# Kernel optimization log

Hardware: AMD Instinct MI355X
Metric: run time of the kernel (lower is better)

Reference implementation:

```python
import jax, jax.numpy as jnp
import numpy as np


def _ternarize(p, delta, w):
    # {-w, 0, +w} via threshold mask, matching TrainableTernarize.forward
    return jnp.where(p > delta, w, jnp.where(p < -delta, -w, jnp.zeros_like(p)))


def _ternary_para(p, w):
    # TrainableTernaryPara.forward: delta = 0.05 * max|p|
    delta = 0.05 * jnp.max(jnp.abs(p))
    return _ternarize(p, delta, w)


def _init_scale(p):
    # w init: mean(|p|[|p| > 0.7 * mean|p|])
    a = jnp.abs(p)
    mask = (a > 0.7 * jnp.mean(a)).astype(p.dtype)
    return jnp.sum(a * mask) / jnp.sum(mask)


def setup_inputs() -> dict:
    key = jax.random.key(0)
    k1, k2, k3 = jax.random.split(key, 3)
    B, S, D_IN, D_OUT = 4, 2048, 4096, 4096
    x = jax.random.normal(k1, (B, S, D_IN), dtype=jnp.float32)
    bound = 1.0 / np.sqrt(D_IN)  # nn.Linear default init range
    W = jax.random.uniform(k2, (D_OUT, D_IN), minval=-bound, maxval=bound, dtype=jnp.float32)
    b = jax.random.uniform(k3, (D_OUT,), minval=-bound, maxval=bound, dtype=jnp.float32)
    w_scale = _init_scale(W)
    b_scale = _init_scale(b)
    return {"x": x, "W": W, "w_scale": w_scale, "b": b, "b_scale": b_scale}


def reference(x, W, w_scale, b, b_scale):
    Wt = _ternary_para(W, w_scale)   # [D_OUT, D_IN] in {-w,0,+w}
    bt = _ternary_para(b, b_scale)   # [D_OUT]
    # F.linear(x, Wt, bt) = x @ Wt.T + bt
    return jnp.einsum('bsi,oi->bso', x, Wt) + bt
```

## Files before the change

kernel.cpp:

```cpp
#include <hip/hip_runtime.h>

typedef int v4i __attribute__((ext_vector_type(4)));

#define BM 128
#define BN 128
#define BK 64

#define GLOAD_LDS(gptr, lptr)                                                         \
  __builtin_amdgcn_global_load_lds(                                                   \
      (const __attribute__((address_space(1))) unsigned int*)(gptr),                  \
      (__attribute__((address_space(3))) unsigned int*)(lptr), 16, 0, 0)


__global__ void absmax2_kernel(const float4* __restrict__ W4, long nW4,
                               const float4* __restrict__ b4, int nb4,
                               unsigned* __restrict__ mx) {
  __shared__ float sm[4];
  float m = 0.f;
  const bool isB = (blockIdx.x == gridDim.x - 1);
  if (!isB) {
    const long stride = (long)(gridDim.x - 1) * blockDim.x;
    for (long i = blockIdx.x * (long)blockDim.x + threadIdx.x; i < nW4; i += stride) {
      float4 v = W4[i];
      m = fmaxf(m, fmaxf(fmaxf(fabsf(v.x), fabsf(v.y)), fmaxf(fabsf(v.z), fabsf(v.w))));
    }
  } else {
    for (int i = threadIdx.x; i < nb4; i += blockDim.x) {
      float4 v = b4[i];
      m = fmaxf(m, fmaxf(fmaxf(fabsf(v.x), fabsf(v.y)), fmaxf(fabsf(v.z), fabsf(v.w))));
    }
  }
  for (int off = 32; off > 0; off >>= 1)
    m = fmaxf(m, __shfl_down(m, off));
  if ((threadIdx.x & 63) == 0) sm[threadIdx.x >> 6] = m;
  __syncthreads();
  if (threadIdx.x == 0) {
    m = fmaxf(fmaxf(sm[0], sm[1]), fmaxf(sm[2], sm[3]));
    atomicMax(mx + (isB ? 1 : 0), __float_as_uint(m));
  }
}

__global__ void xquant_kernel(const float4* __restrict__ X4,
                              signed char* __restrict__ Q,
                              float* __restrict__ sx, int K) {
  __shared__ float sm[4];
  const int row = blockIdx.x;
  const int tid = threadIdx.x;
  const float4* xr = X4 + (size_t)row * (K / 4);
  float4 v[4];
  float m = 0.f;
#pragma unroll
  for (int i = 0; i < 4; ++i) {
    v[i] = xr[tid * 4 + i];
    m = fmaxf(m, fmaxf(fmaxf(fabsf(v[i].x), fabsf(v[i].y)),
                       fmaxf(fabsf(v[i].z), fabsf(v[i].w))));
  }
  for (int off = 32; off > 0; off >>= 1) m = fmaxf(m, __shfl_down(m, off));
  if ((tid & 63) == 0) sm[tid >> 6] = m;
  __syncthreads();
  const float total = fmaxf(fmaxf(sm[0], sm[1]), fmaxf(sm[2], sm[3]));
  const float inv = 127.f / total;
  int wds[4];
#pragma unroll
  for (int i = 0; i < 4; ++i) {
    const float* f = (const float*)&v[i];
    int b[4];
#pragma unroll
    for (int j = 0; j < 4; ++j) {
      float r = rintf(f[j] * inv);
      r = fmaxf(-127.f, fminf(127.f, r));
      b[j] = ((int)r) & 255;
    }
    wds[i] = b[0] | (b[1] << 8) | (b[2] << 16) | (b[3] << 24);
  }
  v4i* out = (v4i*)(Q + (size_t)row * K);
  v4i o = {wds[0], wds[1], wds[2], wds[3]};
  out[tid] = o;
  if (tid == 0) sx[row] = total * (1.f / 127.f);
}

__global__ void prep_w_kernel(const float4* __restrict__ W4, long nW16,
                              const float4* __restrict__ b4, int nb4,
                              const unsigned* __restrict__ mx,
                              const float* __restrict__ bscale,
                              v4i* __restrict__ Tw, float4* __restrict__ bt) {
  if (blockIdx.x == gridDim.x - 1) {
    const float delta = 0.05f * __uint_as_float(mx[1]);
    const float s = *bscale;
    for (int i = threadIdx.x; i < nb4; i += blockDim.x) {
      float4 v = b4[i];
      float4 o;
      o.x = v.x > delta ? s : (v.x < -delta ? -s : 0.f);
      o.y = v.y > delta ? s : (v.y < -delta ? -s : 0.f);
      o.z = v.z > delta ? s : (v.z < -delta ? -s : 0.f);
      o.w = v.w > delta ? s : (v.w < -delta ? -s : 0.f);
      bt[i] = o;
    }
    return;
  }
  long i = blockIdx.x * (long)blockDim.x + threadIdx.x;
  if (i >= nW16) return;
  const float delta = 0.05f * __uint_as_float(mx[0]);
  int wds[4];
#pragma unroll
  for (int u = 0; u < 4; ++u) {
    float4 w = W4[i * 4 + u];
    int b0 = w.x > delta ? 1 : (w.x < -delta ? 0xFF : 0);
    int b1 = w.y > delta ? 1 : (w.y < -delta ? 0xFF : 0);
    int b2 = w.z > delta ? 1 : (w.z < -delta ? 0xFF : 0);
    int b3 = w.w > delta ? 1 : (w.w < -delta ? 0xFF : 0);
    wds[u] = b0 | (b1 << 8) | (b2 << 16) | (b3 << 24);
  }
  v4i o = {wds[0], wds[1], wds[2], wds[3]};
  Tw[i] = o;
}

__global__ __launch_bounds__(256) void gemm_tern_i8(
    const signed char* __restrict__ A,
    const signed char* __restrict__ B,
    const float* __restrict__ sx,
    const float* __restrict__ bt,
    const float* __restrict__ wsc,
    float* __restrict__ C,
    int M, int N, int K) {
  __shared__ __align__(16) signed char sA[BM * BK];
  __shared__ __align__(16) signed char sB[BN * BK];

  const int tid = threadIdx.x;
  const int wave = tid >> 6;
  const int lane = tid & 63;
  const int wm = wave >> 1, wn = wave & 1;
  const int quad = lane >> 4;
  const int l16 = lane & 15;

  const int bm0 = blockIdx.y * BM;
  const int bn0 = blockIdx.x * BN;

  const int srow = tid >> 2;
  const int scol = ((tid & 3) ^ ((tid >> 3) & 3)) * 16;

  const signed char* gA0 = A + (size_t)(bm0 + srow) * K + scol;
  const signed char* gA1 = A + (size_t)(bm0 + 64 + srow) * K + scol;
  const signed char* gB0 = B + (size_t)(bn0 + srow) * K + scol;
  const signed char* gB1 = B + (size_t)(bn0 + 64 + srow) * K + scol;

  signed char* lA0 = sA + (wave * 16) * BK;
  signed char* lA1 = sA + (64 + wave * 16) * BK;
  signed char* lB0 = sB + (wave * 16) * BK;
  signed char* lB1 = sB + (64 + wave * 16) * BK;

  const int kchunk = quad ^ ((l16 >> 1) & 3);
  const v4i* fA = (const v4i*)(sA + (wm * 64 + l16) * BK + kchunk * 16);
  const v4i* fB = (const v4i*)(sB + (wn * 64 + l16) * BK + kchunk * 16);

  v4i acc[4][4] = {};

  for (int k0 = 0; k0 < K; k0 += BK) {
    GLOAD_LDS(gA0, lA0);
    GLOAD_LDS(gA1, lA1);
    GLOAD_LDS(gB0, lB0);
    GLOAD_LDS(gB1, lB1);
    gA0 += BK; gA1 += BK; gB0 += BK; gB1 += BK;
    __syncthreads();

    v4i af[4], bfr[4];
#pragma unroll
    for (int i = 0; i < 4; ++i) af[i] = fA[i * 64];
#pragma unroll
    for (int i = 0; i < 4; ++i) bfr[i] = fB[i * 64];
#pragma unroll
    for (int mt = 0; mt < 4; ++mt)
#pragma unroll
      for (int nt = 0; nt < 4; ++nt)
        acc[mt][nt] = __builtin_amdgcn_mfma_i32_16x16x64_i8(
            af[mt], bfr[nt], acc[mt][nt], 0, 0, 0);
    __syncthreads();
  }

  const float ws = *wsc;
#pragma unroll
  for (int mt = 0; mt < 4; ++mt) {
    const int row = bm0 + wm * 64 + mt * 16 + quad * 4;
    float sc[4];
#pragma unroll
    for (int r = 0; r < 4; ++r) sc[r] = ws * sx[row + r];
#pragma unroll
    for (int nt = 0; nt < 4; ++nt) {
      const int col = bn0 + wn * 64 + nt * 16 + l16;
      const float bias = bt[col];
#pragma unroll
      for (int r = 0; r < 4; ++r)
        C[(size_t)(row + r) * N + col] = sc[r] * (float)acc[mt][nt][r] + bias;
    }
  }
}


extern "C" void kernel_launch(void* const* d_in, const int* in_sizes, int n_in,
                              void* d_out, int out_size, void* d_ws, size_t ws_size,
                              hipStream_t stream) {
  const float* x = (const float*)d_in[0];
  const float* W = (const float*)d_in[1];
  const float* w_scale = (const float*)d_in[2];
  const float* b = (const float*)d_in[3];
  const float* b_scale = (const float*)d_in[4];
  float* out = (float*)d_out;

  const int K = 4096;
  const int N = in_sizes[3];
  const int M = in_sizes[0] / K;

  char* ws = (char*)d_ws;
  signed char* xb = (signed char*)ws;
  signed char* Tw = (signed char*)(ws + (size_t)M * K);
  float* bt = (float*)(ws + (size_t)M * K + (size_t)N * K);
  float* sx = bt + N;
  unsigned* mx = (unsigned*)(sx + M);

  hipMemsetAsync(mx, 0, 8, stream);

  const long nW4 = (long)N * K / 4;
  const int nb4 = N / 4;

  absmax2_kernel<<<1025, 256, 0, stream>>>((const float4*)W, nW4,
                                           (const float4*)b, nb4, mx);

  xquant_kernel<<<M, 256, 0, stream>>>((const float4*)x, xb, sx, K);

  const long nW16 = (long)N * K / 16;
  int gridW = (int)((nW16 + 255) / 256) + 1;
  prep_w_kernel<<<gridW, 256, 0, stream>>>((const float4*)W, nW16,
                                           (const float4*)b, nb4, mx, b_scale,
                                           (v4i*)Tw, (float4*)bt);

  dim3 gg(N / BN, M / BM);
  gemm_tern_i8<<<gg, 256, 0, stream>>>(xb, Tw, sx, bt, w_scale, out, M, N, K);
}
```

Measured before the change: 482.2 us.

## Enlarge GEMM tiles to 256x256 with 4-stage LDS ring prefetch pipeline

The int8 ternary GEMM moves to 256x256 tiles with 512 threads, where each wave computes 128x64. It uses a 4-slot LDS ring that keeps three K-steps of global_load_lds in flight, guarded by a manual vmcnt wait and a barrier, and raises wave priority around the MFMA block. The x-quantization and weight-ternarize kernels switch to coalesced strided access with 4-byte stores, and the weight prep uses a grid-stride loop. The goals are to hide global-load latency behind compute and to raise arithmetic intensity per tile. The costs are higher register and LDS use (128KB LDS) and fewer blocks for the fixed problem size.

```diff
diff --git a/kernel.cpp b/kernel.cpp
--- a/kernel.cpp
+++ b/kernel.cpp
@@ -2,9 +2,10 @@
 
 typedef int v4i __attribute__((ext_vector_type(4)));
 
-#define BM 128
-#define BN 128
-#define BK 64
+#define BM 256
+#define BN 256
+#define BKB 64
+#define NRING 4
 
 #define GLOAD_LDS(gptr, lptr)                                                         \
   __builtin_amdgcn_global_load_lds(                                                   \
@@ -51,7 +52,7 @@
   float m = 0.f;
 #pragma unroll
   for (int i = 0; i < 4; ++i) {
-    v[i] = xr[tid * 4 + i];
+    v[i] = xr[tid + i * 256];
     m = fmaxf(m, fmaxf(fmaxf(fabsf(v[i].x), fabsf(v[i].y)),
                        fmaxf(fabsf(v[i].z), fabsf(v[i].w))));
   }
@@ -60,7 +61,7 @@
   __syncthreads();
   const float total = fmaxf(fmaxf(sm[0], sm[1]), fmaxf(sm[2], sm[3]));
   const float inv = 127.f / total;
-  int wds[4];
+  int* qw = (int*)(Q + (size_t)row * K);
 #pragma unroll
   for (int i = 0; i < 4; ++i) {
     const float* f = (const float*)&v[i];
@@ -71,19 +72,16 @@
       r = fmaxf(-127.f, fminf(127.f, r));
       b[j] = ((int)r) & 255;
     }
-    wds[i] = b[0] | (b[1] << 8) | (b[2] << 16) | (b[3] << 24);
-  }
-  v4i* out = (v4i*)(Q + (size_t)row * K);
-  v4i o = {wds[0], wds[1], wds[2], wds[3]};
-  out[tid] = o;
+    qw[tid + i * 256] = b[0] | (b[1] << 8) | (b[2] << 16) | (b[3] << 24);
+  }
   if (tid == 0) sx[row] = total * (1.f / 127.f);
 }
 
-__global__ void prep_w_kernel(const float4* __restrict__ W4, long nW16,
+__global__ void prep_w_kernel(const float4* __restrict__ W4, long nW4,
                               const float4* __restrict__ b4, int nb4,
                               const unsigned* __restrict__ mx,
                               const float* __restrict__ bscale,
-                              v4i* __restrict__ Tw, float4* __restrict__ bt) {
+                              int* __restrict__ Twi, float4* __restrict__ bt) {
   if (blockIdx.x == gridDim.x - 1) {
     const float delta = 0.05f * __uint_as_float(mx[1]);
     const float s = *bscale;
@@ -98,24 +96,19 @@
     }
     return;
   }
-  long i = blockIdx.x * (long)blockDim.x + threadIdx.x;
-  if (i >= nW16) return;
   const float delta = 0.05f * __uint_as_float(mx[0]);
-  int wds[4];
-#pragma unroll
-  for (int u = 0; u < 4; ++u) {
-    float4 w = W4[i * 4 + u];
+  const long stride = (long)(gridDim.x - 1) * blockDim.x;
+  for (long i = blockIdx.x * (long)blockDim.x + threadIdx.x; i < nW4; i += stride) {
+    float4 w = W4[i];
     int b0 = w.x > delta ? 1 : (w.x < -delta ? 0xFF : 0);
     int b1 = w.y > delta ? 1 : (w.y < -delta ? 0xFF : 0);
     int b2 = w.z > delta ? 1 : (w.z < -delta ? 0xFF : 0);
     int b3 = w.w > delta ? 1 : (w.w < -delta ? 0xFF : 0);
-    wds[u] = b0 | (b1 << 8) | (b2 << 16) | (b3 << 24);
-  }
-  v4i o = {wds[0], wds[1], wds[2], wds[3]};
-  Tw[i] = o;
-}
-
-__global__ __launch_bounds__(256) void gemm_tern_i8(
+    Twi[i] = b0 | (b1 << 8) | (b2 << 16) | (b3 << 24);
+  }
+}
+
+__global__ __launch_bounds__(512, 2) void gemm_tern_i8(
     const signed char* __restrict__ A,
     const signed char* __restrict__ B,
     const float* __restrict__ sx,
@@ -123,64 +116,82 @@
     const float* __restrict__ wsc,
     float* __restrict__ C,
     int M, int N, int K) {
-  __shared__ __align__(16) signed char sA[BM * BK];
-  __shared__ __align__(16) signed char sB[BN * BK];
+  __shared__ __align__(16) signed char lds[NRING][2][BM * BKB];
 
   const int tid = threadIdx.x;
   const int wave = tid >> 6;
   const int lane = tid & 63;
-  const int wm = wave >> 1, wn = wave & 1;
+  const int wm = wave >> 2, wn = wave & 3;
   const int quad = lane >> 4;
   const int l16 = lane & 15;
 
   const int bm0 = blockIdx.y * BM;
   const int bn0 = blockIdx.x * BN;
 
-  const int srow = tid >> 2;
-  const int scol = ((tid & 3) ^ ((tid >> 3) & 3)) * 16;
-
-  const signed char* gA0 = A + (size_t)(bm0 + srow) * K + scol;
-  const signed char* gA1 = A + (size_t)(bm0 + 64 + srow) * K + scol;
-  const signed char* gB0 = B + (size_t)(bn0 + srow) * K + scol;
-  const signed char* gB1 = B + (size_t)(bn0 + 64 + srow) * K + scol;
-
-  signed char* lA0 = sA + (wave * 16) * BK;
-  signed char* lA1 = sA + (64 + wave * 16) * BK;
-  signed char* lB0 = sB + (wave * 16) * BK;
-  signed char* lB1 = sB + (64 + wave * 16) * BK;
+  const signed char* gA[2];
+  const signed char* gB[2];
+#pragma unroll
+  for (int j = 0; j < 2; ++j) {
+    const int idx = j * 512 + tid;
+    const int row = idx >> 2;
+    const int gch = (idx & 3) ^ ((idx >> 3) & 3);
+    gA[j] = A + (size_t)(bm0 + row) * K + gch * 16;
+    gB[j] = B + (size_t)(bn0 + row) * K + gch * 16;
+  }
+  const int ldsbase = wave * 64 * 16;
+
+#define STAGE(slot)                                  \
+  do {                                               \
+    signed char* la = &lds[slot][0][ldsbase];        \
+    signed char* lb = &lds[slot][1][ldsbase];        \
+    GLOAD_LDS(gA[0], la);                            \
+    GLOAD_LDS(gA[1], la + 8192);                     \
+    GLOAD_LDS(gB[0], lb);                            \
+    GLOAD_LDS(gB[1], lb + 8192);                     \
+    gA[0] += BKB; gA[1] += BKB;                      \
+    gB[0] += BKB; gB[1] += BKB;                      \
+  } while (0)
 
   const int kchunk = quad ^ ((l16 >> 1) & 3);
-  const v4i* fA = (const v4i*)(sA + (wm * 64 + l16) * BK + kchunk * 16);
-  const v4i* fB = (const v4i*)(sB + (wn * 64 + l16) * BK + kchunk * 16);
-
-  v4i acc[4][4] = {};
-
-  for (int k0 = 0; k0 < K; k0 += BK) {
-    GLOAD_LDS(gA0, lA0);
-    GLOAD_LDS(gA1, lA1);
-    GLOAD_LDS(gB0, lB0);
-    GLOAD_LDS(gB1, lB1);
-    gA0 += BK; gA1 += BK; gB0 += BK; gB1 += BK;
-    __syncthreads();
-
-    v4i af[4], bfr[4];
-#pragma unroll
-    for (int i = 0; i < 4; ++i) af[i] = fA[i * 64];
-#pragma unroll
-    for (int i = 0; i < 4; ++i) bfr[i] = fB[i * 64];
-#pragma unroll
-    for (int mt = 0; mt < 4; ++mt)
+  const int aoff = (wm * 128 + l16) * BKB + kchunk * 16;
+  const int boff = (wn * 64 + l16) * BKB + kchunk * 16;
+
+  v4i acc[8][4] = {};
+
+  STAGE(0);
+  STAGE(1);
+  STAGE(2);
+  asm volatile("s_waitcnt vmcnt(8)" ::: "memory");
+  asm volatile("s_barrier" ::: "memory");
+
+  const int NT = K / BKB;
+  for (int t = 0; t < NT; ++t) {
+    if (t + 3 < NT) STAGE((t + 3) & 3);
+    const int slot = t & 3;
+    const v4i* fA = (const v4i*)&lds[slot][0][aoff];
+    const v4i* fB = (const v4i*)&lds[slot][1][boff];
+    v4i af[8], bf[4];
+#pragma unroll
+    for (int i = 0; i < 8; ++i) af[i] = fA[i * 64];
+#pragma unroll
+    for (int i = 0; i < 4; ++i) bf[i] = fB[i * 64];
+    __builtin_amdgcn_s_setprio(1);
+#pragma unroll
+    for (int mt = 0; mt < 8; ++mt)
 #pragma unroll
       for (int nt = 0; nt < 4; ++nt)
         acc[mt][nt] = __builtin_amdgcn_mfma_i32_16x16x64_i8(
-            af[mt], bfr[nt], acc[mt][nt], 0, 0, 0);
-    __syncthreads();
-  }
+            af[mt], bf[nt], acc[mt][nt], 0, 0, 0);
+    __builtin_amdgcn_s_setprio(0);
+    asm volatile("s_waitcnt vmcnt(8)" ::: "memory");
+    asm volatile("s_barrier" ::: "memory");
+  }
+#undef STAGE
 
   const float ws = *wsc;
 #pragma unroll
-  for (int mt = 0; mt < 4; ++mt) {
-    const int row = bm0 + wm * 64 + mt * 16 + quad * 4;
+  for (int mt = 0; mt < 8; ++mt) {
+    const int row = bm0 + wm * 128 + mt * 16 + quad * 4;
     float sc[4];
 #pragma unroll
     for (int r = 0; r < 4; ++r) sc[r] = ws * sx[row + r];
@@ -227,12 +238,10 @@
 
   xquant_kernel<<<M, 256, 0, stream>>>((const float4*)x, xb, sx, K);
 
-  const long nW16 = (long)N * K / 16;
-  int gridW = (int)((nW16 + 255) / 256) + 1;
-  prep_w_kernel<<<gridW, 256, 0, stream>>>((const float4*)W, nW16,
-                                           (const float4*)b, nb4, mx, b_scale,
-                                           (v4i*)Tw, (float4*)bt);
+  prep_w_kernel<<<8193, 256, 0, stream>>>((const float4*)W, nW4,
+                                          (const float4*)b, nb4, mx, b_scale,
+                                          (int*)Tw, (float4*)bt);
 
   dim3 gg(N / BN, M / BM);
-  gemm_tern_i8<<<gg, 256, 0, stream>>>(xb, Tw, sx, bt, w_scale, out, M, N, K);
-}
+  gemm_tern_i8<<<gg, 512, 0, stream>>>(xb, Tw, sx, bt, w_scale, out, M, N, K);
+}
```

New measurement: 409.2 us. -15.1%, faster.
